# Kernel optimization log

Hardware: AMD Instinct MI355X
Metric: run time of the kernel (lower is better)

Reference implementation:

```python
import jax, jax.numpy as jnp
import numpy as np

EPS = 1e-8
LN_EPS = 1e-5
B, T, VDIM, ADIM, DM = 8, 2048, 1024, 768, 256
HID = 1024  # max(64, min(4*256, 2048))
DELTA_LOW, DELTA_HIGH = 2.0, 6.0
WINDOW = 5.0
GATE_MIN, GATE_MAX = 0.05, 0.95


def layer_norm(x):
    mu = jnp.mean(x, axis=-1, keepdims=True)
    var = jnp.var(x, axis=-1, keepdims=True)
    return (x - mu) / jnp.sqrt(var + LN_EPS)


def l2_normalize(x):
    n = jnp.sqrt(jnp.sum(x * x, axis=-1, keepdims=True))
    return x / jnp.maximum(n, EPS)


def setup_inputs() -> dict:
    key = jax.random.key(0)
    ks = jax.random.split(key, 8)
    inp = {
        "video_seq": jax.random.normal(ks[0], (B, T, VDIM), jnp.float32),
        "audio_seq": jax.random.normal(ks[1], (B, T, ADIM), jnp.float32),
        "Wv": jax.random.normal(ks[2], (VDIM, DM), jnp.float32) * (1.0 / np.sqrt(VDIM)),
        "bv": jnp.zeros((DM,), jnp.float32),
        "Wa": jax.random.normal(ks[3], (ADIM, DM), jnp.float32) * (1.0 / np.sqrt(ADIM)),
        "ba": jnp.zeros((DM,), jnp.float32),
        "theta": jnp.float32(0.0),
        "W1": jax.random.normal(ks[4], (3 * DM, HID), jnp.float32) * (1.0 / np.sqrt(3 * DM)),
        "b1": jnp.zeros((HID,), jnp.float32),
        "W2": jax.random.normal(ks[5], (HID, 1), jnp.float32) * (1.0 / np.sqrt(HID)),
        "b2": jnp.zeros((1,), jnp.float32),
    }
    return inp


def reference(video_seq, audio_seq, Wv, bv, Wa, ba, theta, W1, b1, W2, b2):
    v = layer_norm(video_seq @ Wv + bv)          # [B,T,DM]
    a = layer_norm(audio_seq @ Wa + ba)          # [B,T,DM]
    b, t, d = v.shape

    # LearnableDelay
    th = jnp.clip(theta, -12.0, 12.0)
    delta = DELTA_LOW + (DELTA_HIGH - DELTA_LOW) * jax.nn.sigmoid(th)
    delta_b = jnp.full((b,), delta, jnp.float32)

    # SoftTemporalShift (right shift with linear interpolation)
    dl = jnp.clip(delta_b, 0.0, float(t - 1))[:, None, None]   # [B,1,1]
    n = jnp.floor(dl)
    alpha = dl - n
    n_i = n.astype(jnp.int32)
    tidx = jnp.arange(t, dtype=jnp.int32)[None, :, None]       # [1,T,1]
    idx0 = jnp.clip(tidx - n_i, 0, t - 1)                      # [B,T,1]
    idx1 = jnp.clip(idx0 + 1, 0, t - 1)
    a0 = jnp.take_along_axis(a, jnp.broadcast_to(idx0, (b, t, d)), axis=1)
    a1 = jnp.take_along_axis(a, jnp.broadcast_to(idx1, (b, t, d)), axis=1)
    a_shift = (1.0 - alpha) * a0 + alpha * a1

    # DisplacementAwareCausalMask (hard, single scale)
    tf = jnp.arange(t, dtype=jnp.float32)
    tt = tf[None, :, None]                                     # t  -> [1,T,1]
    tau = tf[None, None, :]                                    # tau -> [1,1,T]
    center = jnp.minimum(jnp.maximum(tt + delta_b[:, None, None], 0.0), tt)
    raw = (jnp.abs(tau - center) <= WINDOW).astype(jnp.float32)
    raw = raw * (tau <= tt).astype(jnp.float32)
    M = raw / jnp.maximum(jnp.sum(raw, axis=-1, keepdims=True), EPS)  # [B,T,T]

    # mask-weighted audio context
    a_ctx = jnp.einsum('btk,bkd->btd', M, a_shift)

    # AlignmentGate (dropout inactive at eval)
    vn = l2_normalize(v)
    an = l2_normalize(a_ctx)
    x = jnp.concatenate([an, vn, an * vn], axis=-1)            # [B,T,3*DM]
    h = jax.nn.gelu(x @ W1 + b1, approximate=False)
    logits = jnp.clip(h @ W2 + b2, -12.0, 12.0)                # [B,T,1]
    g = jnp.clip(jax.nn.sigmoid(logits), GATE_MIN, GATE_MAX)

    fused = g * a_ctx + (1.0 - g) * v                          # [B,T,DM]
    return fused
```

## Files before the change

kernel.cpp:

```cpp
#include <hip/hip_runtime.h>
#include <cstdint>
#include <cstddef>

typedef unsigned short u16;
typedef unsigned int u32;
typedef __attribute__((ext_vector_type(8))) short short8;
typedef __attribute__((ext_vector_type(4))) float f32x4;

#define T_SEQ 2048
#define BT_ROWS 16384

__device__ __forceinline__ u16 f2bf(float x) {
  union { float f; u32 u; } v; v.f = x;
  u32 r = v.u + 0x7fffu + ((v.u >> 16) & 1u);
  return (u16)(r >> 16);
}
__device__ __forceinline__ u32 pkbf(float lo, float hi) {
  union { float f; u32 u; } a, b; a.f = lo; b.f = hi;
  const u32 ra = a.u + 0x7fffu + ((a.u >> 16) & 1u);
  const u32 rb = b.u + 0x7fffu + ((b.u >> 16) & 1u);
  return __builtin_amdgcn_perm(rb, ra, 0x07060302);
}
__device__ __forceinline__ float wave_bcast_sum(float x) {
#pragma unroll
  for (int off = 32; off > 0; off >>= 1) x += __shfl_down(x, off);
  return __shfl(x, 0);
}
__device__ __forceinline__ void gl_lds16(const void* g, void* l) {
  __builtin_amdgcn_global_load_lds((const __attribute__((address_space(1))) u32*)g,
                                   (__attribute__((address_space(3))) u32*)l, 16, 0, 0);
}
__device__ __forceinline__ float gelu_f(float x) {
  float z = 1.5957691216057308f * x * (1.0f + 0.044715f * x * x);
  float e = __expf(z);
  return x - x * __builtin_amdgcn_rcpf(1.0f + e);
}

__global__ __launch_bounds__(256) void tcvt_all(const float* __restrict__ Wv,
                                                const float* __restrict__ Wa,
                                                const float* __restrict__ W1,
                                                u16* __restrict__ wvT,
                                                u16* __restrict__ waT,
                                                u16* __restrict__ w1T) {
  __shared__ float tile[32][33];
  int b = blockIdx.x;
  const float* in; u16* out; int K, N, bx, by;
  if (b < 256)      { in = Wv; out = wvT; K = 1024; N = 256;  bx = b & 31;  by = b >> 5; }
  else if (b < 448) { b -= 256; in = Wa; out = waT; K = 768; N = 256;  bx = b % 24; by = b / 24; }
  else              { b -= 448; in = W1; out = w1T; K = 768; N = 1024; bx = b % 24; by = b / 24; }
  const int k0 = bx * 32, n0 = by * 32;
  const int tx = threadIdx.x & 31, ty = threadIdx.x >> 5;
#pragma unroll
  for (int r = 0; r < 4; r++)
    tile[ty + r * 8][tx] = in[(size_t)(k0 + ty + r * 8) * N + n0 + tx];
  __syncthreads();
#pragma unroll
  for (int r = 0; r < 4; r++)
    out[(size_t)(n0 + ty + r * 8) * K + k0 + tx] = f2bf(tile[tx][ty + r * 8]);
}

__global__ __launch_bounds__(256, 5) void gemm_proj(const float* __restrict__ Vin,
                                                    const float* __restrict__ Ain,
                                                    const u16* __restrict__ wvT,
                                                    const u16* __restrict__ waT,
                                                    float* __restrict__ Cv,
                                                    float* __restrict__ Ca) {
  __shared__ float Asf[64 * 64];
  __shared__ u16 Bs[128 * 64];
  int b = blockIdx.x;
  const float* A; const u16* Bt; float* C; int K;
  if (b < 512) { A = Vin; Bt = wvT; C = Cv; K = 1024; }
  else         { b -= 512; A = Ain; Bt = waT; C = Ca; K = 768; }
  const int m0 = (b >> 1) * 64;
  const int n0 = (b & 1) * 128;
  const int tid = threadIdx.x;
  const int wave = tid >> 6, lane = tid & 63, qm = lane & 15, quad = lane >> 4;
  const int rw = (wave >> 1) * 32, cw = (wave & 1) * 64;

  const int arow = tid >> 4;
  const int apart = (tid & 15) ^ (arow & 15);
  const float* Ap[4];
#pragma unroll
  for (int g = 0; g < 4; g++)
    Ap[g] = A + (size_t)(m0 + arow + g * 16) * K + apart * 4;
  const int brow = tid >> 3;
  const int bpart = (tid & 7) ^ (brow & 7);
  const u16* Bp[4];
#pragma unroll
  for (int g = 0; g < 4; g++)
    Bp[g] = Bt + (size_t)(n0 + brow + g * 32) * K + bpart * 8;

  f32x4 acc[2][4] = {};
  for (int kt = 0; kt < K; kt += 64) {
#pragma unroll
    for (int g = 0; g < 4; g++) gl_lds16(Ap[g] + kt, &Asf[(tid + g * 256) * 4]);
#pragma unroll
    for (int g = 0; g < 4; g++) gl_lds16(Bp[g] + kt, &Bs[(tid + g * 256) * 8]);
    __syncthreads();
#pragma unroll
    for (int s = 0; s < 2; s++) {
      short8 af[2], bfr[4];
#pragma unroll
      for (int i = 0; i < 2; i++) {
        const int r = rw + i * 16 + qm;
        const int pb = s * 8 + quad * 2;
        const float4 f0 = *(const float4*)&Asf[r * 64 + ((pb) ^ (r & 15)) * 4];
        const float4 f1 = *(const float4*)&Asf[r * 64 + ((pb + 1) ^ (r & 15)) * 4];
        u32 w[4] = {pkbf(f0.x, f0.y), pkbf(f0.z, f0.w), pkbf(f1.x, f1.y), pkbf(f1.z, f1.w)};
        af[i] = *(short8*)w;
      }
#pragma unroll
      for (int j = 0; j < 4; j++) {
        const int r = cw + j * 16 + qm;
        bfr[j] = *(const short8*)&Bs[r * 64 + ((s * 4 + quad) ^ (r & 7)) * 8];
      }
#pragma unroll
      for (int i = 0; i < 2; i++)
#pragma unroll
        for (int j = 0; j < 4; j++)
          acc[i][j] = __builtin_amdgcn_mfma_f32_16x16x32_bf16(af[i], bfr[j], acc[i][j], 0, 0, 0);
    }
    __syncthreads();
  }
#pragma unroll
  for (int i = 0; i < 2; i++) {
    const int row = m0 + rw + i * 16 + quad * 4;
#pragma unroll
    for (int j = 0; j < 4; j++) {
      const int col = n0 + cw + j * 16 + qm;
#pragma unroll
      for (int r = 0; r < 4; r++)
        C[(size_t)(row + r) * 256 + col] = acc[i][j][r];
    }
  }
}

__global__ __launch_bounds__(256, 6) void gemm_gelu_w2(const u16* __restrict__ Axb,
                                                       const u16* __restrict__ Bt,
                                                       const float* __restrict__ b1,
                                                       const float* __restrict__ W2,
                                                       float* __restrict__ logits) {
  constexpr int K = 768;
  __shared__ u16 As[64 * 64];
  __shared__ u16 Bs[128 * 64];
  const int tid = threadIdx.x;
  const int n0 = blockIdx.x * 128;
  const int m0 = blockIdx.y * 64;
  const int wave = tid >> 6, lane = tid & 63, qm = lane & 15, quad = lane >> 4;
  const int rw = (wave >> 1) * 32, cw = (wave & 1) * 64;

  const int crow = tid >> 3;
  const int cpart = (tid & 7) ^ (crow & 7);
  const u16* Ap[2];
#pragma unroll
  for (int g = 0; g < 2; g++)
    Ap[g] = Axb + (size_t)(m0 + crow + g * 32) * K + cpart * 8;
  const u16* Bp[4];
#pragma unroll
  for (int g = 0; g < 4; g++)
    Bp[g] = Bt + (size_t)(n0 + crow + g * 32) * K + cpart * 8;

  f32x4 acc[2][4] = {};
  for (int kt = 0; kt < K; kt += 64) {
#pragma unroll
    for (int g = 0; g < 2; g++) gl_lds16(Ap[g] + kt, &As[(tid + g * 256) * 8]);
#pragma unroll
    for (int g = 0; g < 4; g++) gl_lds16(Bp[g] + kt, &Bs[(tid + g * 256) * 8]);
    __syncthreads();
#pragma unroll
    for (int s = 0; s < 2; s++) {
      short8 af[2], bfr[4];
#pragma unroll
      for (int i = 0; i < 2; i++) {
        const int r = rw + i * 16 + qm;
        af[i] = *(const short8*)&As[r * 64 + ((s * 4 + quad) ^ (r & 7)) * 8];
      }
#pragma unroll
      for (int j = 0; j < 4; j++) {
        const int r = cw + j * 16 + qm;
        bfr[j] = *(const short8*)&Bs[r * 64 + ((s * 4 + quad) ^ (r & 7)) * 8];
      }
#pragma unroll
      for (int i = 0; i < 2; i++)
#pragma unroll
        for (int j = 0; j < 4; j++)
          acc[i][j] = __builtin_amdgcn_mfma_f32_16x16x32_bf16(af[i], bfr[j], acc[i][j], 0, 0, 0);
    }
    __syncthreads();
  }

  float w2j[4], bc[4];
#pragma unroll
  for (int j = 0; j < 4; j++) {
    const int col = n0 + cw + j * 16 + qm;
    w2j[j] = W2[col];
    bc[j] = b1[col];
  }
#pragma unroll
  for (int i = 0; i < 2; i++) {
#pragma unroll
    for (int r = 0; r < 4; r++) {
      float p = 0.0f;
#pragma unroll
      for (int j = 0; j < 4; j++)
        p += gelu_f(acc[i][j][r] + bc[j]) * w2j[j];
      p += __shfl_xor(p, 1);
      p += __shfl_xor(p, 2);
      p += __shfl_xor(p, 4);
      p += __shfl_xor(p, 8);
      if (qm == 0)
        atomicAdd(&logits[m0 + rw + i * 16 + quad * 4 + r], p);
    }
  }
}

__global__ __launch_bounds__(256) void ln2(float* __restrict__ v, float* __restrict__ a,
                                           const float* __restrict__ bv,
                                           const float* __restrict__ ba) {
  const int gr = blockIdx.x * 4 + (threadIdx.x >> 6);
  const int lane = threadIdx.x & 63;
  float* X; const float* bias; int row;
  if (gr < BT_ROWS) { X = v; bias = bv; row = gr; }
  else              { X = a; bias = ba; row = gr - BT_ROWS; }
  float4 x = *(float4*)&X[(size_t)row * 256 + lane * 4];
  const float4 b = *(const float4*)&bias[lane * 4];
  x.x += b.x; x.y += b.y; x.z += b.z; x.w += b.w;
  float s = x.x + x.y + x.z + x.w;
  float s2 = x.x * x.x + x.y * x.y + x.z * x.z + x.w * x.w;
  s = wave_bcast_sum(s);
  s2 = wave_bcast_sum(s2);
  const float mu = s * (1.0f / 256.0f);
  const float var = s2 * (1.0f / 256.0f) - mu * mu;
  const float inv = rsqrtf(var + 1e-5f);
  x.x = (x.x - mu) * inv; x.y = (x.y - mu) * inv;
  x.z = (x.z - mu) * inv; x.w = (x.w - mu) * inv;
  *(float4*)&X[(size_t)row * 256 + lane * 4] = x;
}

__global__ __launch_bounds__(256) void shift_norm(const float* __restrict__ a,
                                                  const float* __restrict__ v,
                                                  float* __restrict__ actx,
                                                  u16* __restrict__ xb,
                                                  const float* __restrict__ theta) {
  const int row = blockIdx.x * 4 + (threadIdx.x >> 6);
  const int lane = threadIdx.x & 63;
  const int d4 = lane * 4;
  const int bb = row >> 11;
  const int t = row & (T_SEQ - 1);
  const float th = fminf(fmaxf(theta[0], -12.0f), 12.0f);
  const float delta = 2.0f + 4.0f * (1.0f / (1.0f + expf(-th)));
  const float dl = fminf(fmaxf(delta, 0.0f), (float)(T_SEQ - 1));
  const float nf = floorf(dl);
  const float alpha = dl - nf;
  const int ni = (int)nf;
  const float center = fminf(fmaxf((float)t + delta, 0.0f), (float)t);
  float sx = 0, sy = 0, sz = 0, sw = 0, cnt = 0.0f;
  const float* ab = a + (size_t)bb * T_SEQ * 256;
#pragma unroll
  for (int j = 0; j < 6; j++) {
    const int tau = t - 5 + j;
    if (tau < 0) continue;
    if (fabsf((float)tau - center) > 5.0f) continue;
    cnt += 1.0f;
    const int i0 = min(max(tau - ni, 0), T_SEQ - 1);
    const int i1 = min(i0 + 1, T_SEQ - 1);
    const float4 a0 = *(const float4*)&ab[(size_t)i0 * 256 + d4];
    const float4 a1 = *(const float4*)&ab[(size_t)i1 * 256 + d4];
    sx += a0.x + alpha * (a1.x - a0.x);
    sy += a0.y + alpha * (a1.y - a0.y);
    sz += a0.z + alpha * (a1.z - a0.z);
    sw += a0.w + alpha * (a1.w - a0.w);
  }
  const float sc = 1.0f / fmaxf(cnt, 1e-8f);
  float4 o; o.x = sx * sc; o.y = sy * sc; o.z = sz * sc; o.w = sw * sc;
  *(float4*)&actx[(size_t)row * 256 + d4] = o;
  const float4 vv = *(const float4*)&v[(size_t)row * 256 + d4];
  float sa2 = o.x * o.x + o.y * o.y + o.z * o.z + o.w * o.w;
  float sv2 = vv.x * vv.x + vv.y * vv.y + vv.z * vv.z + vv.w * vv.w;
  sa2 = wave_bcast_sum(sa2);
  sv2 = wave_bcast_sum(sv2);
  const float ia = 1.0f / fmaxf(sqrtf(sa2), 1e-8f);
  const float iv = 1.0f / fmaxf(sqrtf(sv2), 1e-8f);
  const float anx = o.x * ia, any_ = o.y * ia, anz = o.z * ia, anw = o.w * ia;
  const float vnx = vv.x * iv, vny = vv.y * iv, vnz = vv.z * iv, vnw = vv.w * iv;
  u16* xr = xb + (size_t)row * 768;
  u32 pa[2] = {pkbf(anx, any_), pkbf(anz, anw)};
  u32 pv[2] = {pkbf(vnx, vny), pkbf(vnz, vnw)};
  u32 pp[2] = {pkbf(anx * vnx, any_ * vny), pkbf(anz * vnz, anw * vnw)};
  *(uint2*)&xr[d4] = *(uint2*)pa;
  *(uint2*)&xr[256 + d4] = *(uint2*)pv;
  *(uint2*)&xr[512 + d4] = *(uint2*)pp;
}

__global__ __launch_bounds__(256) void gate_mix(const float* __restrict__ logits,
                                                const float* __restrict__ b2,
                                                const float* __restrict__ actx,
                                                const float* __restrict__ v,
                                                float* __restrict__ out) {
  const int row = blockIdx.x * 4 + (threadIdx.x >> 6);
  const int lane = threadIdx.x & 63;
  const float l = fminf(fmaxf(logits[row] + b2[0], -12.0f), 12.0f);
  float g = 1.0f / (1.0f + expf(-l));
  g = fminf(fmaxf(g, 0.05f), 0.95f);
  const float4 aa = *(const float4*)&actx[(size_t)row * 256 + lane * 4];
  const float4 vv = *(const float4*)&v[(size_t)row * 256 + lane * 4];
  float4 o;
  o.x = g * aa.x + (1.0f - g) * vv.x;
  o.y = g * aa.y + (1.0f - g) * vv.y;
  o.z = g * aa.z + (1.0f - g) * vv.z;
  o.w = g * aa.w + (1.0f - g) * vv.w;
  *(float4*)&out[(size_t)row * 256 + lane * 4] = o;
}

extern "C" void kernel_launch(void* const* d_in, const int* in_sizes, int n_in,
                              void* d_out, int out_size, void* d_ws, size_t ws_size,
                              hipStream_t stream) {
  const float* video = (const float*)d_in[0];
  const float* audio = (const float*)d_in[1];
  const float* Wv    = (const float*)d_in[2];
  const float* bv    = (const float*)d_in[3];
  const float* Wa    = (const float*)d_in[4];
  const float* ba    = (const float*)d_in[5];
  const float* theta = (const float*)d_in[6];
  const float* W1    = (const float*)d_in[7];
  const float* b1    = (const float*)d_in[8];
  const float* W2    = (const float*)d_in[9];
  const float* b2    = (const float*)d_in[10];
  float* out = (float*)d_out;
  char* ws = (char*)d_ws;

  const size_t OFF_WVT = 0;
  const size_t OFF_WAT = 524288;
  const size_t OFF_W1T = 917504;
  const size_t OFF_LOG = 2490368;
  const size_t OFF_V   = 2555904;
  const size_t OFF_A   = 19333120;
  const size_t OFF_ACTX= 36110336;
  const size_t OFF_XB  = 52887552;

  u16* wvT = (u16*)(ws + OFF_WVT);
  u16* waT = (u16*)(ws + OFF_WAT);
  u16* w1T = (u16*)(ws + OFF_W1T);
  float* logits = (float*)(ws + OFF_LOG);
  float* v    = (float*)(ws + OFF_V);
  float* a    = (float*)(ws + OFF_A);
  float* actx = (float*)(ws + OFF_ACTX);
  u16* xb = (u16*)(ws + OFF_XB);

  tcvt_all<<<1216, 256, 0, stream>>>(Wv, Wa, W1, wvT, waT, w1T);
  hipMemsetAsync(logits, 0, BT_ROWS * sizeof(float), stream);
  gemm_proj<<<1024, 256, 0, stream>>>(video, audio, wvT, waT, v, a);
  ln2<<<2 * BT_ROWS / 4, 256, 0, stream>>>(v, a, bv, ba);
  shift_norm<<<BT_ROWS / 4, 256, 0, stream>>>(a, v, actx, xb, theta);
  gemm_gelu_w2<<<dim3(8, BT_ROWS / 64), 256, 0, stream>>>(xb, w1T, b1, W2, logits);
  gate_mix<<<BT_ROWS / 4, 256, 0, stream>>>(logits, b2, actx, v, out);
}
```

Measured before the change: 259.3 us.

## Register-prefetch GEMM tiles instead of direct LDS loads; fold logits memset into convert kernel

```diff
diff --git a/kernel.cpp b/kernel.cpp
--- a/kernel.cpp
+++ b/kernel.cpp
@@ -26,10 +26,6 @@
   for (int off = 32; off > 0; off >>= 1) x += __shfl_down(x, off);
   return __shfl(x, 0);
 }
-__device__ __forceinline__ void gl_lds16(const void* g, void* l) {
-  __builtin_amdgcn_global_load_lds((const __attribute__((address_space(1))) u32*)g,
-                                   (__attribute__((address_space(3))) u32*)l, 16, 0, 0);
-}
 __device__ __forceinline__ float gelu_f(float x) {
   float z = 1.5957691216057308f * x * (1.0f + 0.044715f * x * x);
   float e = __expf(z);
@@ -41,9 +37,14 @@
                                                 const float* __restrict__ W1,
                                                 u16* __restrict__ wvT,
                                                 u16* __restrict__ waT,
-                                                u16* __restrict__ w1T) {
+                                                u16* __restrict__ w1T,
+                                                float* __restrict__ logits) {
+  int b = blockIdx.x;
+  if (b >= 1216) {
+    logits[(b - 1216) * 256 + threadIdx.x] = 0.0f;
+    return;
+  }
   __shared__ float tile[32][33];
-  int b = blockIdx.x;
   const float* in; u16* out; int K, N, bx, by;
   if (b < 256)      { in = Wv; out = wvT; K = 1024; N = 256;  bx = b & 31;  by = b >> 5; }
   else if (b < 448) { b -= 256; in = Wa; out = waT; K = 768; N = 256;  bx = b % 24; by = b / 24; }
@@ -59,7 +60,7 @@
     out[(size_t)(n0 + ty + r * 8) * K + k0 + tx] = f2bf(tile[tx][ty + r * 8]);
 }
 
-__global__ __launch_bounds__(256, 5) void gemm_proj(const float* __restrict__ Vin,
+__global__ __launch_bounds__(256, 4) void gemm_proj(const float* __restrict__ Vin,
                                                     const float* __restrict__ Ain,
                                                     const u16* __restrict__ wvT,
                                                     const u16* __restrict__ waT,
@@ -90,12 +91,24 @@
   for (int g = 0; g < 4; g++)
     Bp[g] = Bt + (size_t)(n0 + brow + g * 32) * K + bpart * 8;
 
+  float4 aReg[4]; uint4 bReg[4];
+#pragma unroll
+  for (int g = 0; g < 4; g++) aReg[g] = *(const float4*)(Ap[g]);
+#pragma unroll
+  for (int g = 0; g < 4; g++) bReg[g] = *(const uint4*)(Bp[g]);
+
   f32x4 acc[2][4] = {};
   for (int kt = 0; kt < K; kt += 64) {
 #pragma unroll
-    for (int g = 0; g < 4; g++) gl_lds16(Ap[g] + kt, &Asf[(tid + g * 256) * 4]);
-#pragma unroll
-    for (int g = 0; g < 4; g++) gl_lds16(Bp[g] + kt, &Bs[(tid + g * 256) * 8]);
+    for (int g = 0; g < 4; g++) *(float4*)&Asf[(tid + g * 256) * 4] = aReg[g];
+#pragma unroll
+    for (int g = 0; g < 4; g++) *(uint4*)&Bs[(tid + g * 256) * 8] = bReg[g];
+    if (kt + 64 < K) {
+#pragma unroll
+      for (int g = 0; g < 4; g++) aReg[g] = *(const float4*)(Ap[g] + kt + 64);
+#pragma unroll
+      for (int g = 0; g < 4; g++) bReg[g] = *(const uint4*)(Bp[g] + kt + 64);
+    }
     __syncthreads();
 #pragma unroll
     for (int s = 0; s < 2; s++) {
@@ -135,7 +148,7 @@
   }
 }
 
-__global__ __launch_bounds__(256, 6) void gemm_gelu_w2(const u16* __restrict__ Axb,
+__global__ __launch_bounds__(256, 4) void gemm_gelu_w2(const u16* __restrict__ Axb,
                                                        const u16* __restrict__ Bt,
                                                        const float* __restrict__ b1,
                                                        const float* __restrict__ W2,
@@ -160,12 +173,24 @@
   for (int g = 0; g < 4; g++)
     Bp[g] = Bt + (size_t)(n0 + crow + g * 32) * K + cpart * 8;
 
+  uint4 aReg[2], bReg[4];
+#pragma unroll
+  for (int g = 0; g < 2; g++) aReg[g] = *(const uint4*)(Ap[g]);
+#pragma unroll
+  for (int g = 0; g < 4; g++) bReg[g] = *(const uint4*)(Bp[g]);
+
   f32x4 acc[2][4] = {};
   for (int kt = 0; kt < K; kt += 64) {
 #pragma unroll
-    for (int g = 0; g < 2; g++) gl_lds16(Ap[g] + kt, &As[(tid + g * 256) * 8]);
-#pragma unroll
-    for (int g = 0; g < 4; g++) gl_lds16(Bp[g] + kt, &Bs[(tid + g * 256) * 8]);
+    for (int g = 0; g < 2; g++) *(uint4*)&As[(tid + g * 256) * 8] = aReg[g];
+#pragma unroll
+    for (int g = 0; g < 4; g++) *(uint4*)&Bs[(tid + g * 256) * 8] = bReg[g];
+    if (kt + 64 < K) {
+#pragma unroll
+      for (int g = 0; g < 2; g++) aReg[g] = *(const uint4*)(Ap[g] + kt + 64);
+#pragma unroll
+      for (int g = 0; g < 4; g++) bReg[g] = *(const uint4*)(Bp[g] + kt + 64);
+    }
     __syncthreads();
 #pragma unroll
     for (int s = 0; s < 2; s++) {
@@ -347,8 +372,7 @@
   float* actx = (float*)(ws + OFF_ACTX);
   u16* xb = (u16*)(ws + OFF_XB);
 
-  tcvt_all<<<1216, 256, 0, stream>>>(Wv, Wa, W1, wvT, waT, w1T);
-  hipMemsetAsync(logits, 0, BT_ROWS * sizeof(float), stream);
+  tcvt_all<<<1280, 256, 0, stream>>>(Wv, Wa, W1, wvT, waT, w1T, logits);
   gemm_proj<<<1024, 256, 0, stream>>>(video, audio, wvT, waT, v, a);
   ln2<<<2 * BT_ROWS / 4, 256, 0, stream>>>(v, a, bv, ba);
   shift_norm<<<BT_ROWS / 4, 256, 0, stream>>>(a, v, actx, xb, theta);
```

After: 626.1 us. 141% more time.

## Load GEMM operands directly from global into registers, fold logits memset into convert kernel

Applied to the files above, without the earlier changes.

```diff
diff --git a/kernel.cpp b/kernel.cpp
--- a/kernel.cpp
+++ b/kernel.cpp
@@ -26,10 +26,6 @@
   for (int off = 32; off > 0; off >>= 1) x += __shfl_down(x, off);
   return __shfl(x, 0);
 }
-__device__ __forceinline__ void gl_lds16(const void* g, void* l) {
-  __builtin_amdgcn_global_load_lds((const __attribute__((address_space(1))) u32*)g,
-                                   (__attribute__((address_space(3))) u32*)l, 16, 0, 0);
-}
 __device__ __forceinline__ float gelu_f(float x) {
   float z = 1.5957691216057308f * x * (1.0f + 0.044715f * x * x);
   float e = __expf(z);
@@ -41,9 +37,14 @@
                                                 const float* __restrict__ W1,
                                                 u16* __restrict__ wvT,
                                                 u16* __restrict__ waT,
-                                                u16* __restrict__ w1T) {
+                                                u16* __restrict__ w1T,
+                                                float* __restrict__ logits) {
+  int b = blockIdx.x;
+  if (b >= 1216) {
+    logits[(b - 1216) * 256 + threadIdx.x] = 0.0f;
+    return;
+  }
   __shared__ float tile[32][33];
-  int b = blockIdx.x;
   const float* in; u16* out; int K, N, bx, by;
   if (b < 256)      { in = Wv; out = wvT; K = 1024; N = 256;  bx = b & 31;  by = b >> 5; }
   else if (b < 448) { b -= 256; in = Wa; out = waT; K = 768; N = 256;  bx = b % 24; by = b / 24; }
@@ -59,14 +60,12 @@
     out[(size_t)(n0 + ty + r * 8) * K + k0 + tx] = f2bf(tile[tx][ty + r * 8]);
 }
 
-__global__ __launch_bounds__(256, 5) void gemm_proj(const float* __restrict__ Vin,
-                                                    const float* __restrict__ Ain,
-                                                    const u16* __restrict__ wvT,
-                                                    const u16* __restrict__ waT,
-                                                    float* __restrict__ Cv,
-                                                    float* __restrict__ Ca) {
-  __shared__ float Asf[64 * 64];
-  __shared__ u16 Bs[128 * 64];
+__global__ __launch_bounds__(256) void gemm_proj(const float* __restrict__ Vin,
+                                                 const float* __restrict__ Ain,
+                                                 const u16* __restrict__ wvT,
+                                                 const u16* __restrict__ waT,
+                                                 float* __restrict__ Cv,
+                                                 float* __restrict__ Ca) {
   int b = blockIdx.x;
   const float* A; const u16* Bt; float* C; int K;
   if (b < 512) { A = Vin; Bt = wvT; C = Cv; K = 1024; }
@@ -77,50 +76,32 @@
   const int wave = tid >> 6, lane = tid & 63, qm = lane & 15, quad = lane >> 4;
   const int rw = (wave >> 1) * 32, cw = (wave & 1) * 64;
 
-  const int arow = tid >> 4;
-  const int apart = (tid & 15) ^ (arow & 15);
-  const float* Ap[4];
-#pragma unroll
-  for (int g = 0; g < 4; g++)
-    Ap[g] = A + (size_t)(m0 + arow + g * 16) * K + apart * 4;
-  const int brow = tid >> 3;
-  const int bpart = (tid & 7) ^ (brow & 7);
-  const u16* Bp[4];
-#pragma unroll
-  for (int g = 0; g < 4; g++)
-    Bp[g] = Bt + (size_t)(n0 + brow + g * 32) * K + bpart * 8;
+  const float* Ar0 = A + (size_t)(m0 + rw + qm) * K + quad * 8;
+  const float* Ar1 = Ar0 + (size_t)16 * K;
+  const u16* Br[4];
+#pragma unroll
+  for (int j = 0; j < 4; j++)
+    Br[j] = Bt + (size_t)(n0 + cw + j * 16 + qm) * K + quad * 8;
 
   f32x4 acc[2][4] = {};
-  for (int kt = 0; kt < K; kt += 64) {
-#pragma unroll
-    for (int g = 0; g < 4; g++) gl_lds16(Ap[g] + kt, &Asf[(tid + g * 256) * 4]);
-#pragma unroll
-    for (int g = 0; g < 4; g++) gl_lds16(Bp[g] + kt, &Bs[(tid + g * 256) * 8]);
-    __syncthreads();
-#pragma unroll
-    for (int s = 0; s < 2; s++) {
-      short8 af[2], bfr[4];
-#pragma unroll
-      for (int i = 0; i < 2; i++) {
-        const int r = rw + i * 16 + qm;
-        const int pb = s * 8 + quad * 2;
-        const float4 f0 = *(const float4*)&Asf[r * 64 + ((pb) ^ (r & 15)) * 4];
-        const float4 f1 = *(const float4*)&Asf[r * 64 + ((pb + 1) ^ (r & 15)) * 4];
-        u32 w[4] = {pkbf(f0.x, f0.y), pkbf(f0.z, f0.w), pkbf(f1.x, f1.y), pkbf(f1.z, f1.w)};
-        af[i] = *(short8*)w;
-      }
-#pragma unroll
-      for (int j = 0; j < 4; j++) {
-        const int r = cw + j * 16 + qm;
-        bfr[j] = *(const short8*)&Bs[r * 64 + ((s * 4 + quad) ^ (r & 7)) * 8];
-      }
-#pragma unroll
-      for (int i = 0; i < 2; i++)
-#pragma unroll
-        for (int j = 0; j < 4; j++)
-          acc[i][j] = __builtin_amdgcn_mfma_f32_16x16x32_bf16(af[i], bfr[j], acc[i][j], 0, 0, 0);
-    }
-    __syncthreads();
+#pragma unroll 2
+  for (int kt = 0; kt < K; kt += 32) {
+    const float4 a00 = *(const float4*)(Ar0 + kt);
+    const float4 a01 = *(const float4*)(Ar0 + kt + 4);
+    const float4 a10 = *(const float4*)(Ar1 + kt);
+    const float4 a11 = *(const float4*)(Ar1 + kt + 4);
+    short8 bfr[4];
+#pragma unroll
+    for (int j = 0; j < 4; j++)
+      bfr[j] = *(const short8*)(Br[j] + kt);
+    u32 w0[4] = {pkbf(a00.x, a00.y), pkbf(a00.z, a00.w), pkbf(a01.x, a01.y), pkbf(a01.z, a01.w)};
+    u32 w1[4] = {pkbf(a10.x, a10.y), pkbf(a10.z, a10.w), pkbf(a11.x, a11.y), pkbf(a11.z, a11.w)};
+    short8 af[2] = {*(short8*)w0, *(short8*)w1};
+#pragma unroll
+    for (int i = 0; i < 2; i++)
+#pragma unroll
+      for (int j = 0; j < 4; j++)
+        acc[i][j] = __builtin_amdgcn_mfma_f32_16x16x32_bf16(af[i], bfr[j], acc[i][j], 0, 0, 0);
   }
 #pragma unroll
   for (int i = 0; i < 2; i++) {
@@ -135,58 +116,40 @@
   }
 }
 
-__global__ __launch_bounds__(256, 6) void gemm_gelu_w2(const u16* __restrict__ Axb,
-                                                       const u16* __restrict__ Bt,
-                                                       const float* __restrict__ b1,
-                                                       const float* __restrict__ W2,
-                                                       float* __restrict__ logits) {
+__global__ __launch_bounds__(256) void gemm_gelu_w2(const u16* __restrict__ Axb,
+                                                    const u16* __restrict__ Bt,
+                                                    const float* __restrict__ b1,
+                                                    const float* __restrict__ W2,
+                                                    float* __restrict__ logits) {
   constexpr int K = 768;
-  __shared__ u16 As[64 * 64];
-  __shared__ u16 Bs[128 * 64];
   const int tid = threadIdx.x;
   const int n0 = blockIdx.x * 128;
   const int m0 = blockIdx.y * 64;
   const int wave = tid >> 6, lane = tid & 63, qm = lane & 15, quad = lane >> 4;
   const int rw = (wave >> 1) * 32, cw = (wave & 1) * 64;
 
-  const int crow = tid >> 3;
-  const int cpart = (tid & 7) ^ (crow & 7);
-  const u16* Ap[2];
-#pragma unroll
-  for (int g = 0; g < 2; g++)
-    Ap[g] = Axb + (size_t)(m0 + crow + g * 32) * K + cpart * 8;
-  const u16* Bp[4];
-#pragma unroll
-  for (int g = 0; g < 4; g++)
-    Bp[g] = Bt + (size_t)(n0 + crow + g * 32) * K + cpart * 8;
+  const u16* Ar0 = Axb + (size_t)(m0 + rw + qm) * K + quad * 8;
+  const u16* Ar1 = Ar0 + (size_t)16 * K;
+  const u16* Br[4];
+#pragma unroll
+  for (int j = 0; j < 4; j++)
+    Br[j] = Bt + (size_t)(n0 + cw + j * 16 + qm) * K + quad * 8;
 
   f32x4 acc[2][4] = {};
-  for (int kt = 0; kt < K; kt += 64) {
-#pragma unroll
-    for (int g = 0; g < 2; g++) gl_lds16(Ap[g] + kt, &As[(tid + g * 256) * 8]);
-#pragma unroll
-    for (int g = 0; g < 4; g++) gl_lds16(Bp[g] + kt, &Bs[(tid + g * 256) * 8]);
-    __syncthreads();
-#pragma unroll
-    for (int s = 0; s < 2; s++) {
-      short8 af[2], bfr[4];
-#pragma unroll
-      for (int i = 0; i < 2; i++) {
-        const int r = rw + i * 16 + qm;
-        af[i] = *(const short8*)&As[r * 64 + ((s * 4 + quad) ^ (r & 7)) * 8];
-      }
-#pragma unroll
-      for (int j = 0; j < 4; j++) {
-        const int r = cw + j * 16 + qm;
-        bfr[j] = *(const short8*)&Bs[r * 64 + ((s * 4 + quad) ^ (r & 7)) * 8];
-      }
-#pragma unroll
-      for (int i = 0; i < 2; i++)
-#pragma unroll
-        for (int j = 0; j < 4; j++)
-          acc[i][j] = __builtin_amdgcn_mfma_f32_16x16x32_bf16(af[i], bfr[j], acc[i][j], 0, 0, 0);
-    }
-    __syncthreads();
+#pragma unroll 2
+  for (int kt = 0; kt < K; kt += 32) {
+    short8 af[2];
+    af[0] = *(const short8*)(Ar0 + kt);
+    af[1] = *(const short8*)(Ar1 + kt);
+    short8 bfr[4];
+#pragma unroll
+    for (int j = 0; j < 4; j++)
+      bfr[j] = *(const short8*)(Br[j] + kt);
+#pragma unroll
+    for (int i = 0; i < 2; i++)
+#pragma unroll
+      for (int j = 0; j < 4; j++)
+        acc[i][j] = __builtin_amdgcn_mfma_f32_16x16x32_bf16(af[i], bfr[j], acc[i][j], 0, 0, 0);
   }
 
   float w2j[4], bc[4];
@@ -347,8 +310,7 @@
   float* actx = (float*)(ws + OFF_ACTX);
   u16* xb = (u16*)(ws + OFF_XB);
 
-  tcvt_all<<<1216, 256, 0, stream>>>(Wv, Wa, W1, wvT, waT, w1T);
-  hipMemsetAsync(logits, 0, BT_ROWS * sizeof(float), stream);
+  tcvt_all<<<1280, 256, 0, stream>>>(Wv, Wa, W1, wvT, waT, w1T, logits);
   gemm_proj<<<1024, 256, 0, stream>>>(video, audio, wvT, waT, v, a);
   ln2<<<2 * BT_ROWS / 4, 256, 0, stream>>>(v, a, bv, ba);
   shift_norm<<<BT_ROWS / 4, 256, 0, stream>>>(a, v, actx, xb, theta);
```

Result: slower. 414.0 us (+59.7%).

## Split projection GEMM over K halves and fold logits memset into conversion kernel

Applied to the files above, without the earlier changes.

```diff
diff --git a/kernel.cpp b/kernel.cpp
--- a/kernel.cpp
+++ b/kernel.cpp
@@ -41,9 +41,14 @@
                                                 const float* __restrict__ W1,
                                                 u16* __restrict__ wvT,
                                                 u16* __restrict__ waT,
-                                                u16* __restrict__ w1T) {
+                                                u16* __restrict__ w1T,
+                                                float* __restrict__ logits) {
+  int b = blockIdx.x;
+  if (b >= 1216) {
+    logits[(b - 1216) * 256 + threadIdx.x] = 0.0f;
+    return;
+  }
   __shared__ float tile[32][33];
-  int b = blockIdx.x;
   const float* in; u16* out; int K, N, bx, by;
   if (b < 256)      { in = Wv; out = wvT; K = 1024; N = 256;  bx = b & 31;  by = b >> 5; }
   else if (b < 448) { b -= 256; in = Wa; out = waT; K = 768; N = 256;  bx = b % 24; by = b / 24; }
@@ -63,16 +68,23 @@
                                                     const float* __restrict__ Ain,
                                                     const u16* __restrict__ wvT,
                                                     const u16* __restrict__ waT,
-                                                    float* __restrict__ Cv,
-                                                    float* __restrict__ Ca) {
+                                                    float* __restrict__ Cv0,
+                                                    float* __restrict__ Cv1,
+                                                    float* __restrict__ Ca0,
+                                                    float* __restrict__ Ca1) {
   __shared__ float Asf[64 * 64];
   __shared__ u16 Bs[128 * 64];
   int b = blockIdx.x;
-  const float* A; const u16* Bt; float* C; int K;
-  if (b < 512) { A = Vin; Bt = wvT; C = Cv; K = 1024; }
-  else         { b -= 512; A = Ain; Bt = waT; C = Ca; K = 768; }
-  const int m0 = (b >> 1) * 64;
-  const int n0 = (b & 1) * 128;
+  const float* A; const u16* Bt; float* C0; float* C1; int K;
+  if (b < 1024) { A = Vin; Bt = wvT; C0 = Cv0; C1 = Cv1; K = 1024; }
+  else          { b -= 1024; A = Ain; Bt = waT; C0 = Ca0; C1 = Ca1; K = 768; }
+  const int kh = b & 1;
+  const int n0 = ((b >> 1) & 1) * 128;
+  const int m0 = (b >> 2) * 64;
+  const int K2 = K >> 1;
+  float* C = kh ? C1 : C0;
+  A += (size_t)kh * K2;
+  Bt += (size_t)kh * K2;
   const int tid = threadIdx.x;
   const int wave = tid >> 6, lane = tid & 63, qm = lane & 15, quad = lane >> 4;
   const int rw = (wave >> 1) * 32, cw = (wave & 1) * 64;
@@ -91,7 +103,7 @@
     Bp[g] = Bt + (size_t)(n0 + brow + g * 32) * K + bpart * 8;
 
   f32x4 acc[2][4] = {};
-  for (int kt = 0; kt < K; kt += 64) {
+  for (int kt = 0; kt < K2; kt += 64) {
 #pragma unroll
     for (int g = 0; g < 4; g++) gl_lds16(Ap[g] + kt, &Asf[(tid + g * 256) * 4]);
 #pragma unroll
@@ -214,17 +226,19 @@
   }
 }
 
-__global__ __launch_bounds__(256) void ln2(float* __restrict__ v, float* __restrict__ a,
+__global__ __launch_bounds__(256) void ln2(float* __restrict__ v0, const float* __restrict__ v1,
+                                           float* __restrict__ a0, const float* __restrict__ a1,
                                            const float* __restrict__ bv,
                                            const float* __restrict__ ba) {
   const int gr = blockIdx.x * 4 + (threadIdx.x >> 6);
   const int lane = threadIdx.x & 63;
-  float* X; const float* bias; int row;
-  if (gr < BT_ROWS) { X = v; bias = bv; row = gr; }
-  else              { X = a; bias = ba; row = gr - BT_ROWS; }
-  float4 x = *(float4*)&X[(size_t)row * 256 + lane * 4];
+  float* X0; const float* X1; const float* bias; int row;
+  if (gr < BT_ROWS) { X0 = v0; X1 = v1; bias = bv; row = gr; }
+  else              { X0 = a0; X1 = a1; bias = ba; row = gr - BT_ROWS; }
+  float4 x = *(float4*)&X0[(size_t)row * 256 + lane * 4];
+  const float4 y = *(const float4*)&X1[(size_t)row * 256 + lane * 4];
   const float4 b = *(const float4*)&bias[lane * 4];
-  x.x += b.x; x.y += b.y; x.z += b.z; x.w += b.w;
+  x.x += y.x + b.x; x.y += y.y + b.y; x.z += y.z + b.z; x.w += y.w + b.w;
   float s = x.x + x.y + x.z + x.w;
   float s2 = x.x * x.x + x.y * x.y + x.z * x.z + x.w * x.w;
   s = wave_bcast_sum(s);
@@ -234,7 +248,7 @@
   const float inv = rsqrtf(var + 1e-5f);
   x.x = (x.x - mu) * inv; x.y = (x.y - mu) * inv;
   x.z = (x.z - mu) * inv; x.w = (x.w - mu) * inv;
-  *(float4*)&X[(size_t)row * 256 + lane * 4] = x;
+  *(float4*)&X0[(size_t)row * 256 + lane * 4] = x;
 }
 
 __global__ __launch_bounds__(256) void shift_norm(const float* __restrict__ a,
@@ -333,24 +347,29 @@
   const size_t OFF_WAT = 524288;
   const size_t OFF_W1T = 917504;
   const size_t OFF_LOG = 2490368;
-  const size_t OFF_V   = 2555904;
-  const size_t OFF_A   = 19333120;
-  const size_t OFF_ACTX= 36110336;
-  const size_t OFF_XB  = 52887552;
+  const size_t OFF_CV0 = 2555904;
+  const size_t OFF_CV1 = 19333120;
+  const size_t OFF_CA0 = 36110336;
+  const size_t OFF_CA1 = 52887552;
+  const size_t OFF_ACTX= 69664768;
+  const size_t OFF_XB  = 86441984;
 
   u16* wvT = (u16*)(ws + OFF_WVT);
   u16* waT = (u16*)(ws + OFF_WAT);
   u16* w1T = (u16*)(ws + OFF_W1T);
   float* logits = (float*)(ws + OFF_LOG);
-  float* v    = (float*)(ws + OFF_V);
-  float* a    = (float*)(ws + OFF_A);
+  float* Cv0  = (float*)(ws + OFF_CV0);
+  float* Cv1  = (float*)(ws + OFF_CV1);
+  float* Ca0  = (float*)(ws + OFF_CA0);
+  float* Ca1  = (float*)(ws + OFF_CA1);
   float* actx = (float*)(ws + OFF_ACTX);
   u16* xb = (u16*)(ws + OFF_XB);
-
-  tcvt_all<<<1216, 256, 0, stream>>>(Wv, Wa, W1, wvT, waT, w1T);
-  hipMemsetAsync(logits, 0, BT_ROWS * sizeof(float), stream);
-  gemm_proj<<<1024, 256, 0, stream>>>(video, audio, wvT, waT, v, a);
-  ln2<<<2 * BT_ROWS / 4, 256, 0, stream>>>(v, a, bv, ba);
+  float* v = Cv0;
+  float* a = Ca0;
+
+  tcvt_all<<<1280, 256, 0, stream>>>(Wv, Wa, W1, wvT, waT, w1T, logits);
+  gemm_proj<<<2048, 256, 0, stream>>>(video, audio, wvT, waT, Cv0, Cv1, Ca0, Ca1);
+  ln2<<<2 * BT_ROWS / 4, 256, 0, stream>>>(Cv0, Cv1, Ca0, Ca1, bv, ba);
   shift_norm<<<BT_ROWS / 4, 256, 0, stream>>>(a, v, actx, xb, theta);
   gemm_gelu_w2<<<dim3(8, BT_ROWS / 64), 256, 0, stream>>>(xb, w1T, b1, W2, logits);
   gate_mix<<<BT_ROWS / 4, 256, 0, stream>>>(logits, b2, actx, v, out);
```

Result: no change. 260.7 us (+0.5%).
